# Performance work log

Measured on AMD Instinct MI355X. Metric: run time of the kernel, lower is better.

## Reference

```python
import jax, jax.numpy as jnp
import numpy as np

H = 8          # attention heads (all three convs)
N_NODES = 50000
N_EDGES = 800000
IN_DIM = 16
N_GRAPHS = 256


def _gat_layer(x, src, dst, W, a_src, a_dst, b, n_nodes):
    """PyG GATConv (concat=True, add_self_loops handled by caller via src/dst)."""
    f_out = a_src.shape[1]
    h = (x @ W).reshape(n_nodes, H, f_out)              # [N,H,F]
    al_s = jnp.einsum('nhf,hf->nh', h, a_src)           # [N,H]
    al_d = jnp.einsum('nhf,hf->nh', h, a_dst)           # [N,H]
    e = jax.nn.leaky_relu(al_s[src] + al_d[dst], 0.2)   # [E,H] per-edge logits
    # segment softmax over incoming edges of each destination node
    m = jax.ops.segment_max(e, dst, num_segments=n_nodes)
    m = jnp.where(jnp.isfinite(m), m, 0.0)
    p = jnp.exp(e - m[dst])
    s = jax.ops.segment_sum(p, dst, num_segments=n_nodes)
    alpha = p / (s[dst] + 1e-16)                        # [E,H]
    out = jax.ops.segment_sum(h[src] * alpha[:, :, None], dst, num_segments=n_nodes)
    return out.reshape(n_nodes, H * f_out) + b


def setup_inputs() -> dict:
    key = jax.random.key(0)
    ks = jax.random.split(key, 16)
    x = jax.random.normal(ks[0], (N_NODES, IN_DIM), dtype=jnp.float32)
    edge_index = jax.random.randint(ks[1], (2, N_EDGES), 0, N_NODES, dtype=jnp.int64)
    batch = jnp.sort(jax.random.randint(ks[2], (N_NODES,), 0, N_GRAPHS, dtype=jnp.int64))

    def glorot(k, shape):
        fan = shape[0] + shape[-1]
        return jax.random.normal(k, shape, dtype=jnp.float32) * np.sqrt(2.0 / fan)

    # conv1: 16 -> 8 heads x 8
    W1 = glorot(ks[3], (IN_DIM, H * 8))
    a_src1 = glorot(ks[4], (H, 8)); a_dst1 = glorot(ks[5], (H, 8))
    b1 = jnp.zeros((H * 8,), jnp.float32)
    # conv2: 64 -> 8 heads x 16
    W2 = glorot(ks[6], (64, H * 16))
    a_src2 = glorot(ks[7], (H, 16)); a_dst2 = glorot(ks[8], (H, 16))
    b2 = jnp.zeros((H * 16,), jnp.float32)
    # conv3: 128 -> 8 heads x 16
    W3 = glorot(ks[9], (128, H * 16))
    a_src3 = glorot(ks[10], (H, 16)); a_dst3 = glorot(ks[11], (H, 16))
    b3 = jnp.zeros((H * 16,), jnp.float32)

    fc1_w = glorot(ks[12], (128, 32)); fc1_b = jnp.zeros((32,), jnp.float32)
    fc2_w = glorot(ks[13], (32, 1));   fc2_b = jnp.zeros((1,), jnp.float32)

    return dict(x=x, edge_index=edge_index, batch=batch,
                W1=W1, a_src1=a_src1, a_dst1=a_dst1, b1=b1,
                W2=W2, a_src2=a_src2, a_dst2=a_dst2, b2=b2,
                W3=W3, a_src3=a_src3, a_dst3=a_dst3, b3=b3,
                fc1_w=fc1_w, fc1_b=fc1_b, fc2_w=fc2_w, fc2_b=fc2_b)


def reference(x, edge_index, batch,
              W1, a_src1, a_dst1, b1,
              W2, a_src2, a_dst2, b2,
              W3, a_src3, a_dst3, b3,
              fc1_w, fc1_b, fc2_w, fc2_b):
    n = x.shape[0]
    loops = jnp.arange(n, dtype=edge_index.dtype)        # GATConv add_self_loops=True
    src = jnp.concatenate([edge_index[0], loops])
    dst = jnp.concatenate([edge_index[1], loops])

    # eval mode: the F.dropout calls are no-ops
    h = jax.nn.elu(_gat_layer(x, src, dst, W1, a_src1, a_dst1, b1, n))
    h = jax.nn.elu(_gat_layer(h, src, dst, W2, a_src2, a_dst2, b2, n))
    h = jax.nn.elu(_gat_layer(h, src, dst, W3, a_src3, a_dst3, b3, n))

    # global_mean_pool over graph ids
    cnt = jax.ops.segment_sum(jnp.ones((n,), h.dtype), batch, num_segments=N_GRAPHS)
    pooled = jax.ops.segment_sum(h, batch, num_segments=N_GRAPHS) / jnp.maximum(cnt, 1.0)[:, None]

    out = jax.nn.relu(pooled @ fc1_w + fc1_b)
    return out @ fc2_w + fc2_b                            # [N_GRAPHS, 1]
```

## Files before the change

kernel.cpp:

```cpp
#include <hip/hip_runtime.h>
#include <hip/hip_bf16.h>
#include <cstdint>
#include <cstddef>

#define GAT_H 8
#define KBMAX 256
#define BCAP  6144
#define SB    8

__device__ __forceinline__ unsigned bf16r(float x) {
    const unsigned u = __float_as_uint(x);
    return (u + 0x7fffu + ((u >> 16) & 1u)) >> 16;
}
#define B2F_LO(u) __uint_as_float((u) << 16)
#define B2F_HI(u) __uint_as_float((u) & 0xffff0000u)


__global__ __launch_bounds__(256) void bkt_scatter(const int* __restrict__ ei,
                                                   int* __restrict__ bwoff,
                                                   unsigned* __restrict__ staging,
                                                   float* __restrict__ Mh,
                                                   int nE, int nN, int kb) {
    __shared__ int cnt[KBMAX];
    __shared__ int gb[KBMAX];
    const int tid = threadIdx.x;
    if (blockIdx.x == 0 && tid < 3 * GAT_H) Mh[tid] = 0.f;
    cnt[tid] = 0;
    __syncthreads();
    const int base = blockIdx.x * 2048;
    const int ET = nE + nN;
    unsigned pk[8]; int bb[8], lr[8];
    #pragma unroll
    for (int k = 0; k < 8; ++k) {
        const int e = base + k * 256 + tid;
        bb[k] = -1;
        if (e < ET) {
            int src, dst;
            if (e < nE) { src = ei[e]; dst = ei[nE + e]; }
            else        { src = dst = e - nE; }
            pk[k] = ((unsigned)dst << 16) | (unsigned)src;
            bb[k] = dst >> 8;
            lr[k] = atomicAdd(&cnt[bb[k]], 1);
        }
    }
    __syncthreads();
    if (tid < kb)
        gb[tid] = cnt[tid] ? atomicAdd(&bwoff[tid], cnt[tid]) : 0;
    __syncthreads();
    #pragma unroll
    for (int k = 0; k < 8; ++k)
        if (bb[k] >= 0) {
            const int pos = gb[bb[k]] + lr[k];
            if (pos < BCAP)
                staging[(size_t)bb[k] * BCAP + pos] = pk[k];
        }
}

__global__ __launch_bounds__(1024) void bkt_build(const unsigned* __restrict__ staging,
                                                  const int* __restrict__ bwoff,
                                                  int* __restrict__ rowptr,
                                                  int* __restrict__ esrc, int N, int kb) {
    __shared__ int hist[256 * SB];
    __shared__ int run[256 * SB];
    __shared__ int sc[KBMAX];
    __shared__ int wt[4];
    __shared__ int wsum[16];
    __shared__ int outv[BCAP];
    const int b = blockIdx.x;
    const int tid = threadIdx.x;
    const int lane = tid & 63, wid = tid >> 6;

    if (tid < KBMAX) sc[tid] = (tid < kb) ? bwoff[tid] : 0;
    for (int i = tid; i < 256 * SB; i += 1024) { hist[i] = 0; run[i] = 0; }
    __syncthreads();

    if (tid < 256) {
        int incl = sc[tid];
        #pragma unroll
        for (int d = 1; d < 64; d <<= 1) {
            const int t2 = __shfl_up(incl, d, 64);
            if (lane >= d) incl += t2;
        }
        if (lane == 63) wt[wid] = incl;
        sc[tid] = incl;
    }
    __syncthreads();
    if (tid < 256) {
        int add = 0;
        #pragma unroll
        for (int w = 0; w < 4; ++w) if (w < wid) add += wt[w];
        sc[tid] += add;
    }
    __syncthreads();
    const int lo   = b ? sc[b - 1] : 0;
    const int cntb = sc[b] - lo;
    const int d0 = b << 8;
    const int nd = min(256, N - d0);
    const unsigned* stg = staging + (size_t)b * BCAP;
    const int lim = min(cntb, BCAP);

    for (int i = tid; i < lim; i += 1024) {
        const unsigned p = stg[i];
        const int dl = (int)(p >> 16) - d0;
        const int q  = (int)(p & 0xffffu) >> 13;
        atomicAdd(&hist[dl * SB + q], 1);
    }
    __syncthreads();

    const int b0 = hist[2 * tid], b1 = hist[2 * tid + 1];
    const int ps = b0 + b1;
    int incl = ps;
    #pragma unroll
    for (int d = 1; d < 64; d <<= 1) {
        const int t2 = __shfl_up(incl, d, 64);
        if (lane >= d) incl += t2;
    }
    if (lane == 63) wsum[wid] = incl;
    __syncthreads();
    if (tid == 0) {
        int runng = 0;
        #pragma unroll
        for (int w = 0; w < 16; ++w) { const int t2 = wsum[w]; wsum[w] = runng; runng += t2; }
    }
    __syncthreads();
    const int excl = wsum[wid] + incl - ps;
    hist[2 * tid]     = excl;
    hist[2 * tid + 1] = excl + b0;
    __syncthreads();

    if (tid < nd)
        rowptr[d0 + tid + 1] = lo + ((tid < 255) ? hist[(tid + 1) * SB] : cntb);
    if (b == 0 && tid == 0) rowptr[0] = 0;

    for (int i = tid; i < lim; i += 1024) {
        const unsigned p = stg[i];
        const int dl = (int)(p >> 16) - d0;
        const int q  = (int)(p & 0xffffu) >> 13;
        const int bin = dl * SB + q;
        const int pos = hist[bin] + atomicAdd(&run[bin], 1);
        if (pos < BCAP) outv[pos] = (int)(p & 0xffffu);
    }
    __syncthreads();
    for (int i = tid; i < lim; i += 1024) esrc[lo + i] = outv[i];
}


template<int D, int C, int KK, int F, typename XT>
__global__ __launch_bounds__(256) void matmul_fused(
        const XT* __restrict__ X, const float* __restrict__ W,
        const float* __restrict__ a_src, const float* __restrict__ a_dst,
        unsigned short* __restrict__ Hb,
        float* __restrict__ als, float* __restrict__ ald,
        float* __restrict__ Mh, int N) {
    constexpr int CG  = C / 8;
    constexpr int NGR = 256 / CG;
    constexpr int NPT = 64 / NGR;
    constexpr int XS  = KK + 4;
    __shared__ float xs[64][XS];
    __shared__ float wsh[KK][C];
    __shared__ float2 phl[64][GAT_H];
    __shared__ int bmax[GAT_H];

    const int n0 = blockIdx.x * 64;
    const int tid = threadIdx.x;
    const int cg = tid % CG, ngr = tid / CG;
    const int c0 = cg * 8;
    if (tid < GAT_H) bmax[tid] = 0;

    float acc[NPT][8];
    #pragma unroll
    for (int i = 0; i < NPT; ++i)
        #pragma unroll
        for (int j = 0; j < 8; ++j) acc[i][j] = 0.f;

    for (int k0 = 0; k0 < D; k0 += KK) {
        if constexpr (sizeof(XT) == 4) {
            for (int t = tid; t < 64 * (KK / 4); t += 256) {
                const int row = t / (KK / 4), c4 = (t % (KK / 4)) * 4;
                const int n = n0 + row;
                float4 v = make_float4(0.f, 0.f, 0.f, 0.f);
                if (n < N) v = *reinterpret_cast<const float4*>(&X[(size_t)n * D + k0 + c4]);
                *reinterpret_cast<float4*>(&xs[row][c4]) = v;
            }
        } else {
            for (int t = tid; t < 64 * (KK / 8); t += 256) {
                const int row = t / (KK / 8), c8 = (t % (KK / 8)) * 8;
                const int n = n0 + row;
                uint4 u = make_uint4(0u, 0u, 0u, 0u);
                if (n < N) u = *reinterpret_cast<const uint4*>(&X[(size_t)n * D + k0 + c8]);
                xs[row][c8 + 0] = B2F_LO(u.x); xs[row][c8 + 1] = B2F_HI(u.x);
                xs[row][c8 + 2] = B2F_LO(u.y); xs[row][c8 + 3] = B2F_HI(u.y);
                xs[row][c8 + 4] = B2F_LO(u.z); xs[row][c8 + 5] = B2F_HI(u.z);
                xs[row][c8 + 6] = B2F_LO(u.w); xs[row][c8 + 7] = B2F_HI(u.w);
            }
        }
        for (int t = tid; t < KK * (C / 4); t += 256) {
            const int row = t / (C / 4), c4 = (t % (C / 4)) * 4;
            *reinterpret_cast<float4*>(&wsh[row][c4]) =
                *reinterpret_cast<const float4*>(&W[(size_t)(k0 + row) * C + c4]);
        }
        __syncthreads();

        #pragma unroll
        for (int k4 = 0; k4 < KK; k4 += 4) {
            float4 xv[NPT];
            #pragma unroll
            for (int i = 0; i < NPT; ++i)
                xv[i] = *reinterpret_cast<const float4*>(&xs[ngr * NPT + i][k4]);
            #pragma unroll
            for (int kk = 0; kk < 4; ++kk) {
                const float4 w0 = *reinterpret_cast<const float4*>(&wsh[k4 + kk][c0]);
                const float4 w1 = *reinterpret_cast<const float4*>(&wsh[k4 + kk][c0 + 4]);
                #pragma unroll
                for (int i = 0; i < NPT; ++i) {
                    const float xk = (kk == 0) ? xv[i].x : (kk == 1) ? xv[i].y
                                   : (kk == 2) ? xv[i].z : xv[i].w;
                    acc[i][0] += xk * w0.x; acc[i][1] += xk * w0.y;
                    acc[i][2] += xk * w0.z; acc[i][3] += xk * w0.w;
                    acc[i][4] += xk * w1.x; acc[i][5] += xk * w1.y;
                    acc[i][6] += xk * w1.z; acc[i][7] += xk * w1.w;
                }
            }
        }
        __syncthreads();
    }

    const int h   = c0 / F;
    const int off = c0 % F;
    float asr[8], adr[8];
    #pragma unroll
    for (int q = 0; q < 8; ++q) {
        asr[q] = a_src[h * F + off + q];
        adr[q] = a_dst[h * F + off + q];
    }

    float ps[NPT], pd[NPT];
    #pragma unroll
    for (int i = 0; i < NPT; ++i) {
        float s = 0.f, d2 = 0.f;
        #pragma unroll
        for (int q = 0; q < 8; ++q) { s += acc[i][q] * asr[q]; d2 += acc[i][q] * adr[q]; }
        ps[i] = s; pd[i] = d2;
        const int n = n0 + ngr * NPT + i;
        if (n < N) {
            uint4 pk;
            pk.x = bf16r(acc[i][0]) | (bf16r(acc[i][1]) << 16);
            pk.y = bf16r(acc[i][2]) | (bf16r(acc[i][3]) << 16);
            pk.z = bf16r(acc[i][4]) | (bf16r(acc[i][5]) << 16);
            pk.w = bf16r(acc[i][6]) | (bf16r(acc[i][7]) << 16);
            *reinterpret_cast<uint4*>(&Hb[(size_t)n * C + c0]) = pk;
        }
    }

    if constexpr (F == 16) {
        if (cg & 1) {
            #pragma unroll
            for (int i = 0; i < NPT; ++i)
                phl[ngr * NPT + i][h] = make_float2(ps[i], pd[i]);
        }
        __syncthreads();
        if (!(cg & 1)) {
            #pragma unroll
            for (int i = 0; i < NPT; ++i) {
                const int nl = ngr * NPT + i;
                const int n = n0 + nl;
                const float al = ps[i] + phl[nl][h].x;
                const float ad = pd[i] + phl[nl][h].y;
                if (n < N) {
                    als[(size_t)n * GAT_H + h] = al;
                    ald[(size_t)n * GAT_H + h] = ad;
                    if (al > 0.f) atomicMax(&bmax[h], __float_as_int(al));
                }
            }
        }
    } else {
        #pragma unroll
        for (int i = 0; i < NPT; ++i) {
            const int n = n0 + ngr * NPT + i;
            if (n < N) {
                als[(size_t)n * GAT_H + h] = ps[i];
                ald[(size_t)n * GAT_H + h] = pd[i];
                if (ps[i] > 0.f) atomicMax(&bmax[h], __float_as_int(ps[i]));
            }
        }
    }
    __syncthreads();
    if (tid < GAT_H) {
        const int v = bmax[tid];
        if (v > 0) atomicMax((int*)&Mh[tid], v);
    }
}


template<int F>
__global__ void gat_gather(const int* __restrict__ rowptr, const int* __restrict__ esrc,
                           const float* __restrict__ als, const float* __restrict__ ald,
                           const float* __restrict__ Mh,
                           const unsigned short* __restrict__ Hb, const float* __restrict__ b,
                           unsigned short* __restrict__ outb, int N) {
    const int t = blockIdx.x * blockDim.x + threadIdx.x;
    if (t >= N * GAT_H) return;
    const int dst = t >> 3, h = t & 7;
    const int beg = rowptr[dst], end = rowptr[dst + 1];
    const float adh = ald[t];
    float bnd = Mh[h] + adh;
    bnd = bnd > 0.f ? bnd : 0.2f * bnd;

    constexpr int NW = F / 2;
    float s = 0.f;
    float acc[F];
    #pragma unroll
    for (int j = 0; j < F; ++j) acc[j] = 0.f;

    int i = beg;
    for (; i + 1 < end; i += 2) {
        const int sa = esrc[i], sb = esrc[i + 1];
        const float ala = als[sa * GAT_H + h];
        const float alb = als[sb * GAT_H + h];
        union { uint4 q[NW / 4]; unsigned w[NW]; } va, vb;
        const uint4* ha  = reinterpret_cast<const uint4*>(Hb + ((size_t)sa * GAT_H + h) * F);
        const uint4* hb2 = reinterpret_cast<const uint4*>(Hb + ((size_t)sb * GAT_H + h) * F);
        #pragma unroll
        for (int j = 0; j < NW / 4; ++j) { va.q[j] = ha[j]; vb.q[j] = hb2[j]; }

        float xa = ala + adh; xa = xa > 0.f ? xa : 0.2f * xa;
        float xb = alb + adh; xb = xb > 0.f ? xb : 0.2f * xb;
        const float pa = __expf(xa - bnd);
        const float pb = __expf(xb - bnd);
        s += pa + pb;
        #pragma unroll
        for (int j = 0; j < NW; ++j) {
            acc[2 * j]     += pa * B2F_LO(va.w[j]) + pb * B2F_LO(vb.w[j]);
            acc[2 * j + 1] += pa * B2F_HI(va.w[j]) + pb * B2F_HI(vb.w[j]);
        }
    }
    if (i < end) {
        const int sa = esrc[i];
        const float ala = als[sa * GAT_H + h];
        union { uint4 q[NW / 4]; unsigned w[NW]; } va;
        const uint4* ha = reinterpret_cast<const uint4*>(Hb + ((size_t)sa * GAT_H + h) * F);
        #pragma unroll
        for (int j = 0; j < NW / 4; ++j) va.q[j] = ha[j];
        float xa = ala + adh; xa = xa > 0.f ? xa : 0.2f * xa;
        const float pa = __expf(xa - bnd);
        s += pa;
        #pragma unroll
        for (int j = 0; j < NW; ++j) {
            acc[2 * j]     += pa * B2F_LO(va.w[j]);
            acc[2 * j + 1] += pa * B2F_HI(va.w[j]);
        }
    }

    const float inv = 1.f / s;
    float val[F];
    #pragma unroll
    for (int j = 0; j < F; ++j) {
        const float v = acc[j] * inv + b[h * F + j];
        val[j] = v > 0.f ? v : expm1f(v);
    }
    #pragma unroll
    for (int j8 = 0; j8 < F / 8; ++j8) {
        uint4 pk;
        pk.x = bf16r(val[8 * j8 + 0]) | (bf16r(val[8 * j8 + 1]) << 16);
        pk.y = bf16r(val[8 * j8 + 2]) | (bf16r(val[8 * j8 + 3]) << 16);
        pk.z = bf16r(val[8 * j8 + 4]) | (bf16r(val[8 * j8 + 5]) << 16);
        pk.w = bf16r(val[8 * j8 + 6]) | (bf16r(val[8 * j8 + 7]) << 16);
        *reinterpret_cast<uint4*>(&outb[((size_t)dst * GAT_H + h) * F + 8 * j8]) = pk;
    }
}


__global__ __launch_bounds__(256) void pool_mlp_kernel(
        const unsigned short* __restrict__ Ab, const int* __restrict__ batch,
        const float* __restrict__ fc1w, const float* __restrict__ fc1b,
        const float* __restrict__ fc2w, const float* __restrict__ fc2b,
        float* __restrict__ out, int N) {
    const int g = blockIdx.x;
    int lo, hi;
    {
        int l = 0, h2 = N;
        while (l < h2) { const int mid = (l + h2) >> 1; if (batch[mid] < g) l = mid + 1; else h2 = mid; }
        lo = l;
        h2 = N;
        while (l < h2) { const int mid = (l + h2) >> 1; if (batch[mid] < g + 1) l = mid + 1; else h2 = mid; }
        hi = l;
    }
    __shared__ float part[16][128];
    __shared__ float pl[128];
    __shared__ float red2[32];
    const int tid = threadIdx.x;
    const int c8 = (tid & 15) * 8, r = tid >> 4;
    float a8[8];
    #pragma unroll
    for (int j = 0; j < 8; ++j) a8[j] = 0.f;
    for (int n = lo + r; n < hi; n += 16) {
        const uint4 u = *reinterpret_cast<const uint4*>(&Ab[(size_t)n * 128 + c8]);
        a8[0] += B2F_LO(u.x); a8[1] += B2F_HI(u.x);
        a8[2] += B2F_LO(u.y); a8[3] += B2F_HI(u.y);
        a8[4] += B2F_LO(u.z); a8[5] += B2F_HI(u.z);
        a8[6] += B2F_LO(u.w); a8[7] += B2F_HI(u.w);
    }
    #pragma unroll
    for (int j = 0; j < 8; ++j) part[r][c8 + j] = a8[j];
    __syncthreads();
    if (tid < 128) {
        float s = 0.f;
        #pragma unroll
        for (int rr = 0; rr < 16; ++rr) s += part[rr][tid];
        pl[tid] = s / fmaxf((float)(hi - lo), 1.f);
    }
    __syncthreads();
    if (tid < 32) {
        float a = fc1b[tid];
        for (int k = 0; k < 128; ++k) a += pl[k] * fc1w[k * 32 + tid];
        a = fmaxf(a, 0.f);
        red2[tid] = a * fc2w[tid];
    }
    __syncthreads();
    if (tid == 0) {
        float sum = fc2b[0];
        for (int k = 0; k < 32; ++k) sum += red2[k];
        out[g] = sum;
    }
}


extern "C" void kernel_launch(void* const* d_in, const int* in_sizes, int n_in,
                              void* d_out, int out_size, void* d_ws, size_t ws_size,
                              hipStream_t stream) {
    const float* x     = (const float*)d_in[0];
    const int*   ei    = (const int*)  d_in[1];
    const int*   batch = (const int*)  d_in[2];
    const float* W1 = (const float*)d_in[3],  *as1 = (const float*)d_in[4],
               *ad1 = (const float*)d_in[5],  *b1  = (const float*)d_in[6];
    const float* W2 = (const float*)d_in[7],  *as2 = (const float*)d_in[8],
               *ad2 = (const float*)d_in[9],  *b2  = (const float*)d_in[10];
    const float* W3 = (const float*)d_in[11], *as3 = (const float*)d_in[12],
               *ad3 = (const float*)d_in[13], *b3  = (const float*)d_in[14];
    const float* fc1w = (const float*)d_in[15], *fc1b = (const float*)d_in[16];
    const float* fc2w = (const float*)d_in[17], *fc2b = (const float*)d_in[18];

    const int N  = in_sizes[0] / 16;
    const int NE = in_sizes[1] / 2;
    const int NG = out_size;
    const int ET = NE + N;
    const int KB = (N + 255) >> 8;

    float* ws = (float*)d_ws;
    size_t off = 0;
    unsigned short* Ab = (unsigned short*)(ws + off); off += (size_t)N * 64;
    unsigned short* Hb = (unsigned short*)(ws + off); off += (size_t)N * 64;
    float* als  = ws + off; off += (size_t)N * GAT_H;
    float* ald  = ws + off; off += (size_t)N * GAT_H;
    float* Mh   = ws + off; off += 3 * GAT_H;
    int* rowptr = (int*)(ws + off); off += N + 1;
    int* esrc   = (int*)(ws + off); off += ET;
    unsigned* staging = (unsigned*)(ws + off); off += (size_t)KB * BCAP;
    int* bwoff  = (int*)(ws + off); off += KBMAX;

    hipMemsetAsync(bwoff, 0, KBMAX * sizeof(int), stream);
    bkt_scatter<<<(ET + 2047) / 2048, 256, 0, stream>>>(ei, bwoff, staging, Mh, NE, N, KB);
    bkt_build<<<KB, 1024, 0, stream>>>(staging, bwoff, rowptr, esrc, N, KB);

    const int NH = N * GAT_H;
    const int NHB = (NH + 255) / 256;
    const int NB = (N + 63) / 64;

    matmul_fused<16, 64, 16, 8, float><<<NB, 256, 0, stream>>>(x, W1, as1, ad1, Hb, als, ald, Mh, N);
    gat_gather<8><<<NHB, 256, 0, stream>>>(rowptr, esrc, als, ald, Mh, Hb, b1, Ab, N);

    matmul_fused<64, 128, 32, 16, unsigned short><<<NB, 256, 0, stream>>>(Ab, W2, as2, ad2, Hb, als, ald, Mh + GAT_H, N);
    gat_gather<16><<<NHB, 256, 0, stream>>>(rowptr, esrc, als, ald, Mh + GAT_H, Hb, b2, Ab, N);

    matmul_fused<128, 128, 32, 16, unsigned short><<<NB, 256, 0, stream>>>(Ab, W3, as3, ad3, Hb, als, ald, Mh + 2 * GAT_H, N);
    gat_gather<16><<<NHB, 256, 0, stream>>>(rowptr, esrc, als, ald, Mh + 2 * GAT_H, Hb, b3, Ab, N);

    pool_mlp_kernel<<<NG, 256, 0, stream>>>(Ab, batch, fc1w, fc1b, fc2w, fc2b,
                                            (float*)d_out, N);
}
```

Baseline: 229.6 us.

## Use bf16 MFMA for layer 2/3 projections with separate attention-logit kernel

Replaces the scalar fp32 FMA matmul for conv2 and conv3 with a bf16 MFMA 16x16x32 kernel. The weights are pre-transposed and converted to bf16 on device. Attention logits and the per-head max move into a new kernel that reads back the bf16 H output. This cuts ALU time in the matmul, but adds two extra kernel launches per layer plus an extra read of H, and the logits are now computed from bf16-rounded features.

```diff
diff --git a/kernel.cpp b/kernel.cpp
--- a/kernel.cpp
+++ b/kernel.cpp
@@ -7,6 +7,9 @@
 #define KBMAX 256
 #define BCAP  6144
 #define SB    8
+
+typedef short bf16x8 __attribute__((ext_vector_type(8)));
+typedef float f32x4  __attribute__((ext_vector_type(4)));
 
 __device__ __forceinline__ unsigned bf16r(float x) {
     const unsigned u = __float_as_uint(x);
@@ -145,9 +148,110 @@
 }
 
 
-template<int D, int C, int KK, int F, typename XT>
+__global__ void wconv_kernel(const float* __restrict__ W, unsigned short* __restrict__ Wt, int D) {
+    const int t = blockIdx.x * blockDim.x + threadIdx.x;
+    if (t >= 128 * D) return;
+    const int c = t / D, k = t % D;
+    Wt[t] = (unsigned short)bf16r(W[(size_t)k * 128 + c]);
+}
+
+
+template<int D>
+__global__ __launch_bounds__(256) void matmul_mfma(
+        const unsigned short* __restrict__ X,
+        const unsigned short* __restrict__ Wt,
+        unsigned short* __restrict__ Hb,
+        int N) {
+    constexpr int DP = D + 8;
+    __shared__ unsigned short xs[64 * DP];
+    __shared__ unsigned short wsh[128 * DP];
+    const int tid = threadIdx.x;
+    const int n0 = blockIdx.x * 64;
+
+    for (int t = tid; t < 64 * (D / 8); t += 256) {
+        const int row = t / (D / 8), c8 = (t % (D / 8)) * 8;
+        const int n = n0 + row;
+        uint4 u = make_uint4(0u, 0u, 0u, 0u);
+        if (n < N) u = *reinterpret_cast<const uint4*>(&X[(size_t)n * D + c8]);
+        *reinterpret_cast<uint4*>(&xs[row * DP + c8]) = u;
+    }
+    for (int t = tid; t < 128 * (D / 8); t += 256) {
+        const int row = t / (D / 8), c8 = (t % (D / 8)) * 8;
+        *reinterpret_cast<uint4*>(&wsh[row * DP + c8]) =
+            *reinterpret_cast<const uint4*>(&Wt[(size_t)row * D + c8]);
+    }
+    __syncthreads();
+
+    const int w = tid >> 6, l = tid & 63;
+    const int lr = l & 15, lk = l >> 4;
+    f32x4 acc[8];
+    #pragma unroll
+    for (int j = 0; j < 8; ++j) acc[j] = (f32x4){0.f, 0.f, 0.f, 0.f};
+
+    #pragma unroll
+    for (int ks = 0; ks < D / 32; ++ks) {
+        const int kb = ks * 32 + lk * 8;
+        const bf16x8 a = *reinterpret_cast<const bf16x8*>(&xs[(16 * w + lr) * DP + kb]);
+        #pragma unroll
+        for (int nt = 0; nt < 8; ++nt) {
+            const bf16x8 bfr = *reinterpret_cast<const bf16x8*>(&wsh[(16 * nt + lr) * DP + kb]);
+            acc[nt] = __builtin_amdgcn_mfma_f32_16x16x32_bf16(a, bfr, acc[nt], 0, 0, 0);
+        }
+    }
+
+    #pragma unroll
+    for (int nt = 0; nt < 8; ++nt) {
+        #pragma unroll
+        for (int r = 0; r < 4; ++r) {
+            const int n = n0 + 16 * w + lk * 4 + r;
+            if (n < N)
+                Hb[(size_t)n * 128 + 16 * nt + lr] = (unsigned short)bf16r(acc[nt][r]);
+        }
+    }
+}
+
+
+__global__ __launch_bounds__(256) void attnlogit_kernel(
+        const unsigned short* __restrict__ Hb,
+        const float* __restrict__ a_src, const float* __restrict__ a_dst,
+        float* __restrict__ als, float* __restrict__ ald,
+        float* __restrict__ Mh, int N) {
+    __shared__ float sh[256];
+    const int t = blockIdx.x * 256 + threadIdx.x;
+    const int tid = threadIdx.x;
+    float s1 = -1e30f;
+    if (t < N * GAT_H) {
+        const int h = t & 7;
+        union { uint4 q[2]; unsigned w[8]; } v;
+        const uint4* hp = reinterpret_cast<const uint4*>(Hb + (size_t)t * 16);
+        v.q[0] = hp[0]; v.q[1] = hp[1];
+        float a1 = 0.f, a2 = 0.f;
+        #pragma unroll
+        for (int j = 0; j < 8; ++j) {
+            const float lo = B2F_LO(v.w[j]), hi2 = B2F_HI(v.w[j]);
+            a1 += lo * a_src[h * 16 + 2 * j] + hi2 * a_src[h * 16 + 2 * j + 1];
+            a2 += lo * a_dst[h * 16 + 2 * j] + hi2 * a_dst[h * 16 + 2 * j + 1];
+        }
+        als[t] = a1; ald[t] = a2;
+        s1 = a1;
+    }
+    sh[tid] = s1;
+    __syncthreads();
+    #pragma unroll
+    for (int off = 128; off >= 8; off >>= 1) {
+        if (tid < off) sh[tid] = fmaxf(sh[tid], sh[tid + off]);
+        __syncthreads();
+    }
+    if (tid < 8) {
+        const float v2 = sh[tid];
+        if (v2 > 0.f) atomicMax((int*)&Mh[tid], __float_as_int(v2));
+    }
+}
+
+
+template<int D, int C, int KK, int F>
 __global__ __launch_bounds__(256) void matmul_fused(
-        const XT* __restrict__ X, const float* __restrict__ W,
+        const float* __restrict__ X, const float* __restrict__ W,
         const float* __restrict__ a_src, const float* __restrict__ a_dst,
         unsigned short* __restrict__ Hb,
         float* __restrict__ als, float* __restrict__ ald,
@@ -158,7 +262,6 @@
     constexpr int XS  = KK + 4;
     __shared__ float xs[64][XS];
     __shared__ float wsh[KK][C];
-    __shared__ float2 phl[64][GAT_H];
     __shared__ int bmax[GAT_H];
 
     const int n0 = blockIdx.x * 64;
@@ -174,25 +277,12 @@
         for (int j = 0; j < 8; ++j) acc[i][j] = 0.f;
 
     for (int k0 = 0; k0 < D; k0 += KK) {
-        if constexpr (sizeof(XT) == 4) {
-            for (int t = tid; t < 64 * (KK / 4); t += 256) {
-                const int row = t / (KK / 4), c4 = (t % (KK / 4)) * 4;
-                const int n = n0 + row;
-                float4 v = make_float4(0.f, 0.f, 0.f, 0.f);
-                if (n < N) v = *reinterpret_cast<const float4*>(&X[(size_t)n * D + k0 + c4]);
-                *reinterpret_cast<float4*>(&xs[row][c4]) = v;
-            }
-        } else {
-            for (int t = tid; t < 64 * (KK / 8); t += 256) {
-                const int row = t / (KK / 8), c8 = (t % (KK / 8)) * 8;
-                const int n = n0 + row;
-                uint4 u = make_uint4(0u, 0u, 0u, 0u);
-                if (n < N) u = *reinterpret_cast<const uint4*>(&X[(size_t)n * D + k0 + c8]);
-                xs[row][c8 + 0] = B2F_LO(u.x); xs[row][c8 + 1] = B2F_HI(u.x);
-                xs[row][c8 + 2] = B2F_LO(u.y); xs[row][c8 + 3] = B2F_HI(u.y);
-                xs[row][c8 + 4] = B2F_LO(u.z); xs[row][c8 + 5] = B2F_HI(u.z);
-                xs[row][c8 + 6] = B2F_LO(u.w); xs[row][c8 + 7] = B2F_HI(u.w);
-            }
+        for (int t = tid; t < 64 * (KK / 4); t += 256) {
+            const int row = t / (KK / 4), c4 = (t % (KK / 4)) * 4;
+            const int n = n0 + row;
+            float4 v = make_float4(0.f, 0.f, 0.f, 0.f);
+            if (n < N) v = *reinterpret_cast<const float4*>(&X[(size_t)n * D + k0 + c4]);
+            *reinterpret_cast<float4*>(&xs[row][c4]) = v;
         }
         for (int t = tid; t < KK * (C / 4); t += 256) {
             const int row = t / (C / 4), c4 = (t % (C / 4)) * 4;
@@ -226,21 +316,18 @@
     }
 
     const int h   = c0 / F;
-    const int off = c0 % F;
     float asr[8], adr[8];
     #pragma unroll
     for (int q = 0; q < 8; ++q) {
-        asr[q] = a_src[h * F + off + q];
-        adr[q] = a_dst[h * F + off + q];
-    }
-
-    float ps[NPT], pd[NPT];
+        asr[q] = a_src[h * F + q];
+        adr[q] = a_dst[h * F + q];
+    }
+
     #pragma unroll
     for (int i = 0; i < NPT; ++i) {
         float s = 0.f, d2 = 0.f;
         #pragma unroll
         for (int q = 0; q < 8; ++q) { s += acc[i][q] * asr[q]; d2 += acc[i][q] * adr[q]; }
-        ps[i] = s; pd[i] = d2;
         const int n = n0 + ngr * NPT + i;
         if (n < N) {
             uint4 pk;
@@ -249,39 +336,9 @@
             pk.z = bf16r(acc[i][4]) | (bf16r(acc[i][5]) << 16);
             pk.w = bf16r(acc[i][6]) | (bf16r(acc[i][7]) << 16);
             *reinterpret_cast<uint4*>(&Hb[(size_t)n * C + c0]) = pk;
-        }
-    }
-
-    if constexpr (F == 16) {
-        if (cg & 1) {
-            #pragma unroll
-            for (int i = 0; i < NPT; ++i)
-                phl[ngr * NPT + i][h] = make_float2(ps[i], pd[i]);
-        }
-        __syncthreads();
-        if (!(cg & 1)) {
-            #pragma unroll
-            for (int i = 0; i < NPT; ++i) {
-                const int nl = ngr * NPT + i;
-                const int n = n0 + nl;
-                const float al = ps[i] + phl[nl][h].x;
-                const float ad = pd[i] + phl[nl][h].y;
-                if (n < N) {
-                    als[(size_t)n * GAT_H + h] = al;
-                    ald[(size_t)n * GAT_H + h] = ad;
-                    if (al > 0.f) atomicMax(&bmax[h], __float_as_int(al));
-                }
-            }
-        }
-    } else {
-        #pragma unroll
-        for (int i = 0; i < NPT; ++i) {
-            const int n = n0 + ngr * NPT + i;
-            if (n < N) {
-                als[(size_t)n * GAT_H + h] = ps[i];
-                ald[(size_t)n * GAT_H + h] = pd[i];
-                if (ps[i] > 0.f) atomicMax(&bmax[h], __float_as_int(ps[i]));
-            }
+            als[(size_t)n * GAT_H + h] = s;
+            ald[(size_t)n * GAT_H + h] = d2;
+            if (s > 0.f) atomicMax(&bmax[h], __float_as_int(s));
         }
     }
     __syncthreads();
@@ -457,22 +514,28 @@
     int* esrc   = (int*)(ws + off); off += ET;
     unsigned* staging = (unsigned*)(ws + off); off += (size_t)KB * BCAP;
     int* bwoff  = (int*)(ws + off); off += KBMAX;
+    unsigned short* Wt2 = (unsigned short*)(ws + off); off += 128 * 64 / 2;
+    unsigned short* Wt3 = (unsigned short*)(ws + off); off += 128 * 128 / 2;
 
     hipMemsetAsync(bwoff, 0, KBMAX * sizeof(int), stream);
     bkt_scatter<<<(ET + 2047) / 2048, 256, 0, stream>>>(ei, bwoff, staging, Mh, NE, N, KB);
     bkt_build<<<KB, 1024, 0, stream>>>(staging, bwoff, rowptr, esrc, N, KB);
+    wconv_kernel<<<(128 * 64 + 255) / 256, 256, 0, stream>>>(W2, Wt2, 64);
+    wconv_kernel<<<(128 * 128 + 255) / 256, 256, 0, stream>>>(W3, Wt3, 128);
 
     const int NH = N * GAT_H;
     const int NHB = (NH + 255) / 256;
     const int NB = (N + 63) / 64;
 
-    matmul_fused<16, 64, 16, 8, float><<<NB, 256, 0, stream>>>(x, W1, as1, ad1, Hb, als, ald, Mh, N);
+    matmul_fused<16, 64, 16, 8><<<NB, 256, 0, stream>>>(x, W1, as1, ad1, Hb, als, ald, Mh, N);
     gat_gather<8><<<NHB, 256, 0, stream>>>(rowptr, esrc, als, ald, Mh, Hb, b1, Ab, N);
 
-    matmul_fused<64, 128, 32, 16, unsigned short><<<NB, 256, 0, stream>>>(Ab, W2, as2, ad2, Hb, als, ald, Mh + GAT_H, N);
+    matmul_mfma<64><<<NB, 256, 0, stream>>>(Ab, Wt2, Hb, N);
+    attnlogit_kernel<<<NHB, 256, 0, stream>>>(Hb, as2, ad2, als, ald, Mh + GAT_H, N);
     gat_gather<16><<<NHB, 256, 0, stream>>>(rowptr, esrc, als, ald, Mh + GAT_H, Hb, b2, Ab, N);
 
-    matmul_fused<128, 128, 32, 16, unsigned short><<<NB, 256, 0, stream>>>(Ab, W3, as3, ad3, Hb, als, ald, Mh + 2 * GAT_H, N);
+    matmul_mfma<128><<<NB, 256, 0, stream>>>(Ab, Wt3, Hb, N);
+    attnlogit_kernel<<<NHB, 256, 0, stream>>>(Hb, as3, ad3, als, ald, Mh + 2 * GAT_H, N);
     gat_gather<16><<<NHB, 256, 0, stream>>>(rowptr, esrc, als, ald, Mh + 2 * GAT_H, Hb, b3, Ab, N);
 
     pool_mlp_kernel<<<NG, 256, 0, stream>>>(Ab, batch, fc1w, fc1b, fc2w, fc2b,
```

New measurement: 233.1 us. About the same (+1.5%).
